# Optimization experiments

Hardware: AMD Instinct MI355X
Metric: run time of the kernel (lower is better)

## Reference

```python
import jax, jax.numpy as jnp
import numpy as np

EPS_COV = 1e-5


def svd_whiten(x):
    # x: (N, C, H, W) -> whitened (N, C, H*W), whitening matrix (N, C, C), mean (N, C, 1)
    N, C, H, W = x.shape
    xf = x.reshape(N, C, H * W)
    mean = xf.mean(-1, keepdims=True)
    xc = xf - mean
    cov = jnp.einsum('nch,ndh->ncd', xc, xc) / (H * W - 1) + EPS_COV * jnp.eye(C, dtype=x.dtype)
    # SVD of symmetric PSD cov; wm = U diag(e^-1/2) U^T (sign-invariant)
    u, e, _ = jnp.linalg.svd(cov)
    wm = jnp.einsum('nij,nj,nkj->nik', u, 1.0 / jnp.sqrt(e), u)
    whitened = jnp.einsum('ncd,ndh->nch', wm, xc)
    return whitened, wm, mean


def randomize_texture(wm, eps):
    # wm: (B, C, C); eps: (B, C, C) standard normal noise
    B, C, _ = wm.shape
    eye = jnp.eye(C, dtype=wm.dtype)
    triu_mask = jnp.triu(jnp.ones((C, C), dtype=wm.dtype))  # includes diagonal
    wm_trid = wm * (1.0 - triu_mask)  # strictly lower triangle, zeros elsewhere
    num_tri = C * (C - 1) / 2.0
    trid_mean = wm_trid.sum((1, 2)) / num_tri  # (B,)
    # NOTE: faithful to source -- the (C*C - num_tri) structural zeros contribute
    # (0 - mean)^2 terms, and divisor is num_tri.
    trid_std = jnp.sqrt(((wm_trid - trid_mean[:, None, None]) ** 2).sum((1, 2)) / num_tri)
    wm_samp = trid_mean[:, None, None] + 10.0 * trid_std[:, None, None] * eps  # torch.normal(mean, 10*std)
    triu_new = wm_samp * triu_mask
    trid_new = jnp.swapaxes(triu_new, 1, 2)
    diag_new = jnp.diagonal(wm_samp, axis1=1, axis2=2)  # (B, C)
    diag_orig = jnp.diagonal(wm, axis1=1, axis2=2)
    wm_new = triu_new + trid_new - 2.0 * eye * diag_new[:, :, None] + eye * diag_orig[:, :, None]
    return wm_new


def reference(x, eps):
    N, C, H, W = x.shape
    # avg_pool2d(x, 2) then nearest upsample back to (H, W): exact 2x2 block mean repeat
    pooled = x.reshape(N, C, H // 2, 2, W // 2, 2).mean(axis=(3, 5))
    up = jnp.repeat(jnp.repeat(pooled, 2, axis=2), 2, axis=3)
    HH = x - up
    LL = up
    cont_min = jnp.min(LL)
    cont_max = jnp.max(LL)
    whiten_cF, wm_c, c_mean = svd_whiten(LL)
    wm_s = randomize_texture(wm_c, eps)
    # torch.bmm(torch.inverse(wm_s), whiten_cF) == solve(wm_s, whiten_cF)
    target = jnp.linalg.solve(wm_s, whiten_cF)  # (N, C, H*W)
    target = target.reshape(N, C, H, W) + c_mean.reshape(N, C, 1, 1)
    target = jnp.clip(target, cont_min, cont_max)
    return HH + target


def setup_inputs() -> dict:
    key = jax.random.key(0)
    k1, k2 = jax.random.split(key)
    x = jax.random.normal(k1, (8, 256, 128, 128), dtype=jnp.float32)
    eps = jax.random.normal(k2, (8, 256, 256), dtype=jnp.float32)
    return {"x": x, "eps": eps}
```

## Files before the change

kernel.cpp:

```cpp
#include <hip/hip_runtime.h>
#include <math.h>

#define N_B   8
#define C_DIM 256
#define H_DIM 128
#define W_DIM 128
#define HW    (H_DIM*W_DIM)
#define PH    64
#define PW    64
#define PHW   (PH*PW)
#define CC    (C_DIM*C_DIM)
#define EPS_COV 1e-5f
#define COVSCALE (4.0f / 16383.0f)
#define NBGJ 16
#define PGLD 33

__device__ inline unsigned int fenc(float f) {
    unsigned int u = __float_as_uint(f);
    return (u & 0x80000000u) ? ~u : (u | 0x80000000u);
}
__device__ inline float fdec(unsigned int u) {
    return (u & 0x80000000u) ? __uint_as_float(u & 0x7fffffffu) : __uint_as_float(~u);
}

__global__ void pool_kernel(const float* __restrict__ x, float* __restrict__ p,
                            float* __restrict__ mean, float* __restrict__ sqb,
                            unsigned int* __restrict__ mm)
{
    int nc = blockIdx.x;
    int t  = threadIdx.x;
    const float* xp = x + (size_t)nc * HW;
    float* pp = p + (size_t)nc * PHW;
    float lsum = 0.f, lsq = 0.f, lmin = 1e30f, lmax = -1e30f;
    #pragma unroll
    for (int i = 0; i < PHW/256; ++i) {
        int pidx = i*256 + t;
        int ph = pidx >> 6, pw = pidx & 63;
        const float* r0 = xp + (size_t)(2*ph)*W_DIM + 2*pw;
        float2 a = *reinterpret_cast<const float2*>(r0);
        float2 b = *reinterpret_cast<const float2*>(r0 + W_DIM);
        float v = (a.x + a.y + b.x + b.y) * 0.25f;
        pp[pidx] = v;
        lsum += v;
        lsq  += v * v;
        lmin = fminf(lmin, v);
        lmax = fmaxf(lmax, v);
    }
    __shared__ float ssum[256], ssq[256], smin[256], smax[256];
    ssum[t] = lsum; ssq[t] = lsq; smin[t] = lmin; smax[t] = lmax;
    __syncthreads();
    for (int s = 128; s > 0; s >>= 1) {
        if (t < s) {
            ssum[t] += ssum[t+s];
            ssq[t]  += ssq[t+s];
            smin[t] = fminf(smin[t], smin[t+s]);
            smax[t] = fmaxf(smax[t], smax[t+s]);
        }
        __syncthreads();
    }
    if (t == 0) {
        mean[nc] = ssum[0] / (float)PHW;
        sqb[nc]  = ssq[0];
        atomicMin(&mm[0], fenc(smin[0]));
        atomicMax(&mm[1], fenc(smax[0]));
    }
}

__global__ void cvec_kernel(const float* __restrict__ mean, const float* __restrict__ sqb,
                            float* __restrict__ cvec, float* __restrict__ scv)
{
    int b = blockIdx.x, t = threadIdx.x;
    float m = mean[b*C_DIM + t];
    float s2 = sqb[b*C_DIM + t];
    float cv = COVSCALE * (s2 - (float)PHW * m * m) + EPS_COV;
    __shared__ float s[256];
    s[t] = cv; __syncthreads();
    for (int st = 128; st > 0; st >>= 1) {
        if (t < st) s[t] += s[t+st];
        __syncthreads();
    }
    if (t == 0) {
        float c = s[0] / 256.0f;
        cvec[b] = c;
        scv[b] = 1.0f / sqrtf(c);
    }
}

__global__ void cov_part_kernel(const float* __restrict__ p, const float* __restrict__ mean,
                                float* __restrict__ c0p, float* __restrict__ c1p,
                                float* __restrict__ c2p, float* __restrict__ c3p)
{
    int bx = blockIdx.x, by = blockIdx.y;
    if (bx > by) return;
    int bz = blockIdx.z;
    int b  = bz >> 2, ks = bz & 3;
    float* covp = (ks == 0) ? c0p : (ks == 1) ? c1p : (ks == 2) ? c2p : c3p;
    int c0 = bx * 64, d0 = by * 64;
    int t  = threadIdx.x;
    int tx = t & 15, ty = t >> 4;
    __shared__ float As[16][68];
    __shared__ float Bs[16][68];
    const float* pb = p + (size_t)b * C_DIM * PHW;
    const float* mb = mean + b * C_DIM;
    int lr  = t >> 2;
    int lc4 = (t & 3) * 4;
    float am = mb[c0 + lr];
    float bm = mb[d0 + lr];
    const float* aptr = pb + (size_t)(c0 + lr) * PHW + ks*1024 + lc4;
    const float* bptr = pb + (size_t)(d0 + lr) * PHW + ks*1024 + lc4;
    float acc[4][4] = {};
    for (int k0 = 0; k0 < 1024; k0 += 16) {
        float4 av = *reinterpret_cast<const float4*>(aptr + k0);
        float4 bv = *reinterpret_cast<const float4*>(bptr + k0);
        __syncthreads();
        As[lc4+0][lr] = av.x - am; As[lc4+1][lr] = av.y - am;
        As[lc4+2][lr] = av.z - am; As[lc4+3][lr] = av.w - am;
        Bs[lc4+0][lr] = bv.x - bm; Bs[lc4+1][lr] = bv.y - bm;
        Bs[lc4+2][lr] = bv.z - bm; Bs[lc4+3][lr] = bv.w - bm;
        __syncthreads();
        #pragma unroll
        for (int kk = 0; kk < 16; ++kk) {
            float4 a4 = *reinterpret_cast<const float4*>(&As[kk][ty*4]);
            float4 b4 = *reinterpret_cast<const float4*>(&Bs[kk][tx*4]);
            float a[4] = {a4.x, a4.y, a4.z, a4.w};
            float bb[4] = {b4.x, b4.y, b4.z, b4.w};
            #pragma unroll
            for (int i = 0; i < 4; ++i)
                #pragma unroll
                for (int j = 0; j < 4; ++j)
                    acc[i][j] += a[i] * bb[j];
        }
    }
    float* cb = covp + (size_t)b * CC;
    #pragma unroll
    for (int i = 0; i < 4; ++i) {
        int ci = c0 + ty*4 + i;
        #pragma unroll
        for (int j = 0; j < 4; ++j) {
            int dj = d0 + tx*4 + j;
            cb[(size_t)ci * C_DIM + dj] = acc[i][j];
            cb[(size_t)dj * C_DIM + ci] = acc[i][j];
        }
    }
}

__global__ void combine_kernel(const float* __restrict__ c0p, const float* __restrict__ c1p,
                               const float* __restrict__ c2p, const float* __restrict__ c3p,
                               const float* __restrict__ cvec,
                               float* __restrict__ Y, float* __restrict__ W0)
{
    size_t idx = (size_t)blockIdx.x * 256 + threadIdx.x;
    int b  = (int)(idx >> 16);
    int ij = (int)(idx & 65535);
    int diag = ((ij >> 8) == (ij & 255));
    float s = (c0p[idx] + c1p[idx] + c2p[idx] + c3p[idx]) * COVSCALE;
    float covv = s + (diag ? EPS_COV : 0.0f);
    float y = covv * (1.0f / cvec[b]);
    Y[idx] = y;
    W0[idx] = (diag ? 1.5f : 0.0f) - 0.5f * y;
}

__device__ inline void tile64(const float* __restrict__ Ab, int lda,
                              const float* __restrict__ Bb, int ldb,
                              int n, int r0, int c0, int t,
                              float (&As)[16][68], float (&Bs)[16][68],
                              float (&acc)[4][4])
{
    int tx = t & 15, ty = t >> 4;
    int lr = t >> 2, lc4 = (t & 3) * 4;
    int brow = t >> 4, bcol = (t & 15) * 4;
    for (int k0 = 0; k0 < n; k0 += 16) {
        float4 av = *reinterpret_cast<const float4*>(Ab + (size_t)(r0+lr)*lda + k0 + lc4);
        float4 bv = *reinterpret_cast<const float4*>(Bb + (size_t)(k0+brow)*ldb + c0 + bcol);
        __syncthreads();
        As[lc4+0][lr] = av.x; As[lc4+1][lr] = av.y; As[lc4+2][lr] = av.z; As[lc4+3][lr] = av.w;
        *reinterpret_cast<float4*>(&Bs[brow][bcol]) = bv;
        __syncthreads();
        #pragma unroll
        for (int kk = 0; kk < 16; ++kk) {
            float4 a4 = *reinterpret_cast<const float4*>(&As[kk][ty*4]);
            float4 b4 = *reinterpret_cast<const float4*>(&Bs[kk][tx*4]);
            float a[4] = {a4.x, a4.y, a4.z, a4.w};
            float bb[4] = {b4.x, b4.y, b4.z, b4.w};
            #pragma unroll
            for (int i = 0; i < 4; ++i)
                #pragma unroll
                for (int j = 0; j < 4; ++j)
                    acc[i][j] += a[i] * bb[j];
        }
    }
}

__global__ void gemm_kernel(const float* __restrict__ A, int lda, long long sA,
                            const float* __restrict__ B, int ldb, long long sB,
                            float* __restrict__ C, int ldc, long long sC,
                            const float* __restrict__ Cin, int ldcin, long long sCin,
                            const float* __restrict__ alphav,
                            int n, float alpha, float beta, float gamma)
{
    int b  = blockIdx.z;
    int r0 = blockIdx.x * 64, c0 = blockIdx.y * 64;
    int t  = threadIdx.x;
    int tx = t & 15, ty = t >> 4;
    __shared__ float As[16][68];
    __shared__ float Bs[16][68];
    float acc[4][4] = {};
    tile64(A + (size_t)b*sA, lda, B + (size_t)b*sB, ldb, n, r0, c0, t, As, Bs, acc);
    float al = alpha * (alphav ? alphav[b] : 1.0f);
    float* Cb = C + (size_t)b * sC;
    #pragma unroll
    for (int i = 0; i < 4; ++i) {
        int r = r0 + ty*4 + i;
        #pragma unroll
        for (int j = 0; j < 4; ++j) {
            int c = c0 + tx*4 + j;
            float v = al * acc[i][j];
            if (beta != 0.0f && r == c) v += beta;
            if (gamma != 0.0f) v += gamma * Cin[(size_t)b*sCin + (size_t)r*ldcin + c];
            Cb[(size_t)r*ldc + c] = v;
        }
    }
}

__global__ void ns_pair_kernel(const float* __restrict__ Y, const float* __restrict__ Z,
                               const float* __restrict__ W,
                               float* __restrict__ Yn, float* __restrict__ Zn)
{
    int bz = blockIdx.z;
    int b = bz >> 1, which = bz & 1;
    const float* A = which ? W + (size_t)b*CC : Y + (size_t)b*CC;
    const float* B = which ? Z + (size_t)b*CC : W + (size_t)b*CC;
    float*       C = which ? Zn + (size_t)b*CC : Yn + (size_t)b*CC;
    int r0 = blockIdx.x * 64, c0 = blockIdx.y * 64;
    int t  = threadIdx.x;
    int tx = t & 15, ty = t >> 4;
    __shared__ float As[16][68];
    __shared__ float Bs[16][68];
    float acc[4][4] = {};
    tile64(A, 256, B, 256, 256, r0, c0, t, As, Bs, acc);
    #pragma unroll
    for (int i = 0; i < 4; ++i)
        #pragma unroll
        for (int j = 0; j < 4; ++j)
            C[(size_t)(r0+ty*4+i)*256 + c0+tx*4+j] = acc[i][j];
}

__global__ void tex_partial_kernel(const float* __restrict__ Zf,
                                   float* __restrict__ tsum, float* __restrict__ tsq)
{
    int bx = blockIdx.x;
    int b = bx >> 5, chunk = bx & 31;
    const float* w = Zf + (size_t)b * CC;
    int t = threadIdx.x;
    int base = chunk * 2048;
    float sum = 0.f, sq = 0.f;
    #pragma unroll
    for (int k = 0; k < 8; ++k) {
        int flat = base + k*256 + t;
        int i = flat >> 8, j = flat & 255;
        if (i > j) {
            float v = w[flat];
            sum += v; sq += v * v;
        }
    }
    __shared__ float s1[256], s2[256];
    s1[t] = sum; s2[t] = sq;
    __syncthreads();
    for (int st = 128; st > 0; st >>= 1) {
        if (t < st) { s1[t] += s1[t+st]; s2[t] += s2[t+st]; }
        __syncthreads();
    }
    if (t == 0) {
        atomicAdd(&tsum[b], s1[0]);
        atomicAdd(&tsq[b],  s2[0]);
    }
}

__global__ void assemble_kernel(const float* __restrict__ Zf, const float* __restrict__ scv,
                                const float* __restrict__ eps,
                                const float* __restrict__ tsum, const float* __restrict__ tsq,
                                float* __restrict__ wms)
{
    size_t idx = (size_t)blockIdx.x * 256 + threadIdx.x;
    int b  = (int)(idx >> 16);
    int ij = (int)(idx & 65535);
    int i = ij >> 8, j = ij & 255;
    float s = scv[b];
    float v;
    if (i == j) {
        v = Zf[idx] * s;
    } else {
        float sum = tsum[b] * s;
        float sq  = tsq[b] * s * s;
        float m = sum / 32640.0f;
        float var = (sq - 2.0f*m*sum + m*m*65536.0f) / 32640.0f;
        float sd = sqrtf(fmaxf(var, 0.0f));
        int lo = min(i, j), hi = max(i, j);
        v = m + 10.0f * sd * eps[(size_t)b*CC + (size_t)lo*256 + hi];
    }
    wms[idx] = v;
}

__global__ __launch_bounds__(256, 1)
void gj_inv128_kernel(const float* __restrict__ Ain, int lda, long long sA,
                      float* __restrict__ Out, int ldo, long long sO)
{
    __shared__ float PG[2][128][PGLD];
    __shared__ float Rs[NBGJ][256];
    __shared__ int   pivots[NBGJ];
    __shared__ int   rowdest[128];
    __shared__ int   used[128];
    __shared__ float sh_rp;
    __shared__ int   sh_p;

    int b = blockIdx.x;
    int t = threadIdx.x;
    int q = t & 15;
    int rg = t >> 4;
    const float* Ab = Ain + (size_t)b * sA;

    float Areg[8][16];
    #pragma unroll
    for (int rr = 0; rr < 8; ++rr) {
        int r = rg*8 + rr;
        #pragma unroll
        for (int cc = 0; cc < 16; ++cc) {
            int c = q + cc*16;
            Areg[rr][cc] = (c < 128) ? Ab[(size_t)r*lda + c]
                                     : ((c - 128 == r) ? 1.0f : 0.0f);
        }
    }
    if (t < 128) used[t] = 0;
    __syncthreads();

    for (int pb = 0; pb < 8; ++pb) {
        #pragma unroll
        for (int rr = 0; rr < 8; ++rr) {
            float val = 0.f;
            #pragma unroll
            for (int cc = 0; cc < 16; ++cc)
                if (cc == pb) val = Areg[rr][cc];
            PG[0][rg*8 + rr][q] = val;
            PG[0][rg*8 + rr][16 + q] = 0.f;
        }
        __syncthreads();

        #pragma unroll
        for (int j = 0; j < NBGJ; ++j) {
            const int cur = j & 1;
            if (t < 64) {
                float v1 = used[t]    ? -1.f : fabsf(PG[cur][t][j]);
                float v2 = used[t+64] ? -1.f : fabsf(PG[cur][t+64][j]);
                int i1 = t;
                if (v2 > v1) { v1 = v2; i1 = t + 64; }
                #pragma unroll
                for (int m = 32; m; m >>= 1) {
                    float ov = __shfl_xor(v1, m);
                    int   oi = __shfl_xor(i1, m);
                    if (ov > v1) { v1 = ov; i1 = oi; }
                }
                if (t == 0) {
                    sh_p = i1;
                    sh_rp = 1.0f / PG[cur][i1][j];
                    pivots[j] = i1;
                    rowdest[i1] = pb*NBGJ + j;
                    used[i1] = 1;
                }
            }
            __syncthreads();
            if (t < 128) {
                int p = sh_p; float rp = sh_rp;
                float f = PG[cur][t][j];
                float v = (t == p) ? (rp - 1.0f) : (-f * rp);
                #pragma unroll
                for (int jj = 0; jj < 32; ++jj) {
                    float nv = fmaf(v, PG[cur][p][jj], PG[cur][t][jj]);
                    PG[cur^1][t][jj] = (jj == 16 + j) ? v : nv;
                }
            }
            __syncthreads();
        }

        for (int j = 0; j < NBGJ; ++j) {
            int p = pivots[j];
            if ((p >> 3) == rg) {
                #pragma unroll
                for (int rr = 0; rr < 8; ++rr)
                    if ((p & 7) == rr) {
                        #pragma unroll
                        for (int cc = 0; cc < 16; ++cc)
                            Rs[j][q + cc*16] = Areg[rr][cc];
                    }
            }
        }
        __syncthreads();

        #pragma unroll
        for (int j = 0; j < NBGJ; ++j) {
            float rv[16];
            #pragma unroll
            for (int cc = 0; cc < 16; ++cc) rv[cc] = Rs[j][q + cc*16];
            #pragma unroll
            for (int rr = 0; rr < 8; ++rr) {
                float g = PG[0][rg*8 + rr][16 + j];
                #pragma unroll
                for (int cc = 0; cc < 16; ++cc)
                    Areg[rr][cc] = fmaf(g, rv[cc], Areg[rr][cc]);
            }
        }
        __syncthreads();
    }

    float* Ob = Out + (size_t)b * sO;
    #pragma unroll
    for (int rr = 0; rr < 8; ++rr) {
        int r = rg*8 + rr;
        int dest = rowdest[r];
        #pragma unroll
        for (int cc = 8; cc < 16; ++cc) {
            int c = q + cc*16;
            Ob[(size_t)dest*ldo + (c - 128)] = Areg[rr][cc];
        }
    }
}

__global__ void transpose128_kernel(const float* __restrict__ In, float* __restrict__ Outp)
{
    __shared__ float tile[16][17];
    int b = blockIdx.z;
    int r0 = blockIdx.y * 16, c0 = blockIdx.x * 16;
    int t = threadIdx.x;
    int tx = t & 15, ty = t >> 4;
    tile[ty][tx] = In[(size_t)b*CC + (size_t)(r0+ty)*256 + c0+tx];
    __syncthreads();
    Outp[(size_t)b*CC + (size_t)(c0+ty)*256 + r0+tx] = tile[tx][ty];
}

__global__ void target_kernel(const float* __restrict__ M, const float* __restrict__ p,
                              const float* __restrict__ mean, const float* __restrict__ x,
                              const unsigned int* __restrict__ mm, float* __restrict__ out)
{
    int b  = blockIdx.z;
    int c0 = blockIdx.x * 64;
    int ph = blockIdx.y;
    int h0 = ph * 64;
    int t  = threadIdx.x;
    int tx = t & 15, ty = t >> 4;
    __shared__ float As[16][68];
    __shared__ float Bs[16][68];
    __shared__ float accS[64][66];
    const float* Mb = M + (size_t)b * CC;
    const float* pb = p + (size_t)b * C_DIM * PHW;
    const float* mb = mean + b * C_DIM;
    int lr   = t >> 2;
    int lc4  = (t & 3) * 4;
    int brow = t >> 4;
    int bcol = (t & 15) * 4;
    float acc[4][4] = {};
    for (int k0 = 0; k0 < C_DIM; k0 += 16) {
        float4 av = *reinterpret_cast<const float4*>(Mb + (size_t)(c0+lr)*C_DIM + k0 + lc4);
        float  bm = mb[k0 + brow];
        float4 bv = *reinterpret_cast<const float4*>(pb + (size_t)(k0+brow)*PHW + h0 + bcol);
        bv.x -= bm; bv.y -= bm; bv.z -= bm; bv.w -= bm;
        __syncthreads();
        As[lc4+0][lr] = av.x; As[lc4+1][lr] = av.y; As[lc4+2][lr] = av.z; As[lc4+3][lr] = av.w;
        *reinterpret_cast<float4*>(&Bs[brow][bcol]) = bv;
        __syncthreads();
        #pragma unroll
        for (int kk = 0; kk < 16; ++kk) {
            float4 a4 = *reinterpret_cast<const float4*>(&As[kk][ty*4]);
            float4 b4 = *reinterpret_cast<const float4*>(&Bs[kk][tx*4]);
            float a[4] = {a4.x, a4.y, a4.z, a4.w};
            float bb[4] = {b4.x, b4.y, b4.z, b4.w};
            #pragma unroll
            for (int i = 0; i < 4; ++i)
                #pragma unroll
                for (int j = 0; j < 4; ++j)
                    acc[i][j] += a[i] * bb[j];
        }
    }
    __syncthreads();
    #pragma unroll
    for (int i = 0; i < 4; ++i)
        *reinterpret_cast<float4*>(&accS[ty*4+i][tx*4]) =
            make_float4(acc[i][0], acc[i][1], acc[i][2], acc[i][3]);
    __syncthreads();
    float mn = fdec(mm[0]);
    float mx = fdec(mm[1]);
    int lane_ch = t >> 5;
    int col4 = (t & 31) * 4;
    int pw2 = (t & 31) * 2;
    #pragma unroll
    for (int cc8 = 0; cc8 < 64; cc8 += 8) {
        int ch  = cc8 + lane_ch;
        int gch = c0 + ch;
        float me = mb[gch];
        float2 av = *reinterpret_cast<const float2*>(&accS[ch][pw2]);
        float t0 = fminf(fmaxf(av.x + me, mn), mx);
        float t1 = fminf(fmaxf(av.y + me, mn), mx);
        float2 pv = *reinterpret_cast<const float2*>(
            pb + (size_t)gch * PHW + h0 + pw2);
        size_t xbase = (((size_t)b * C_DIM + gch) * H_DIM + 2*ph) * W_DIM + col4;
        #pragma unroll
        for (int row = 0; row < 2; ++row) {
            float4 xv = *reinterpret_cast<const float4*>(x + xbase + row*W_DIM);
            float4 o;
            o.x = xv.x - pv.x + t0;
            o.y = xv.y - pv.x + t0;
            o.z = xv.z - pv.y + t1;
            o.w = xv.w - pv.y + t1;
            *reinterpret_cast<float4*>(out + xbase + row*W_DIM) = o;
        }
    }
}

extern "C" void kernel_launch(void* const* d_in, const int* in_sizes, int n_in,
                              void* d_out, int out_size, void* d_ws, size_t ws_size,
                              hipStream_t stream)
{
    const float* x   = (const float*)d_in[0];
    const float* eps = (const float*)d_in[1];
    float* out = (float*)d_out;
    float* w = (float*)d_ws;

    size_t o = 0;
    float* p    = w + o; o += (size_t)N_B * C_DIM * PHW;
    float* bufA = w + o; o += (size_t)N_B * CC;
    float* bufY = w + o; o += (size_t)N_B * CC;
    float* bufZ = w + o; o += (size_t)N_B * CC;
    float* bufY2= w + o; o += (size_t)N_B * CC;
    float* bufZ2= w + o; o += (size_t)N_B * CC;
    float* bufW = w + o; o += (size_t)N_B * CC;
    float* bufT = w + o; o += (size_t)N_B * CC;
    float* meanb= w + o; o += N_B * C_DIM;
    float* sqb  = w + o; o += N_B * C_DIM;
    float* cvec = w + o; o += N_B;
    float* scv  = w + o; o += N_B;
    float* tsum = w + o; o += N_B;
    float* tsq  = w + o; o += N_B;
    unsigned int* mmx = (unsigned int*)(w + o); o += 2;

    float* wms  = bufA;
    float* covp0 = bufY2, *covp1 = bufZ, *covp2 = bufZ2, *covp3 = bufT;
    float* invA11 = bufW;
    float* T1     = bufW + (size_t)N_B * 128 * 128;
    float* Sm     = bufW + (size_t)N_B * 128 * 128 * 2;
    float* Minv   = bufY2;
    float* Rb     = bufZ;
    float* Minv2  = bufY;
    float* Mm     = bufT;

    hipMemsetAsync(mmx,     0xFF, 4, stream);
    hipMemsetAsync(mmx + 1, 0x00, 4, stream);
    hipMemsetAsync(tsum, 0, 2 * N_B * sizeof(float), stream);

    pool_kernel<<<N_B * C_DIM, 256, 0, stream>>>(x, p, meanb, sqb, mmx);
    cvec_kernel<<<N_B, 256, 0, stream>>>(meanb, sqb, cvec, scv);
    cov_part_kernel<<<dim3(4, 4, N_B*4), 256, 0, stream>>>(p, meanb, covp0, covp1, covp2, covp3);
    combine_kernel<<<2048, 256, 0, stream>>>(covp0, covp1, covp2, covp3, cvec, bufY, bufW);

    const long long S  = (long long)CC;
    const long long Sh = 128LL * 128LL;

    gemm_kernel<<<dim3(4,4,N_B), 256, 0, stream>>>(bufY,256,S, bufW,256,S, bufY2,256,S,
                                                   nullptr,0,0, nullptr, 256, 1.0f, 0.0f, 0.0f);
    gemm_kernel<<<dim3(4,4,N_B), 256, 0, stream>>>(bufW,256,S, bufY2,256,S, bufY,256,S,
                                                   nullptr,0,0, nullptr, 256, -0.5f, 1.5f, 0.0f);
    ns_pair_kernel<<<dim3(4,4,2*N_B), 256, 0, stream>>>(bufY2, bufW, bufY, bufZ, bufZ2);
    gemm_kernel<<<dim3(4,4,N_B), 256, 0, stream>>>(bufZ2,256,S, bufZ,256,S, bufY2,256,S,
                                                   nullptr,0,0, nullptr, 256, -0.5f, 1.5f, 0.0f);
    ns_pair_kernel<<<dim3(4,4,2*N_B), 256, 0, stream>>>(bufZ, bufZ2, bufY2, bufW, bufY);
    gemm_kernel<<<dim3(4,4,N_B), 256, 0, stream>>>(bufY,256,S, bufW,256,S, bufZ,256,S,
                                                   nullptr,0,0, nullptr, 256, -0.5f, 1.5f, 0.0f);
    gemm_kernel<<<dim3(4,4,N_B), 256, 0, stream>>>(bufZ,256,S, bufY,256,S, bufZ2,256,S,
                                                   nullptr,0,0, nullptr, 256, 1.0f, 0.0f, 0.0f);

    tex_partial_kernel<<<256, 256, 0, stream>>>(bufZ2, tsum, tsq);
    assemble_kernel<<<2048, 256, 0, stream>>>(bufZ2, scv, eps, tsum, tsq, wms);

    gj_inv128_kernel<<<N_B, 256, 0, stream>>>(wms, 256, S, invA11, 128, Sh);
    gemm_kernel<<<dim3(2,2,N_B), 256, 0, stream>>>(invA11,128,Sh, wms+128,256,S, T1,128,Sh,
                                                   nullptr,0,0, nullptr, 128, 1.0f, 0.0f, 0.0f);
    gemm_kernel<<<dim3(2,2,N_B), 256, 0, stream>>>(wms+128*256,256,S, T1,128,Sh, Sm,128,Sh,
                                                   wms+128*256+128,256,S, nullptr, 128, -1.0f, 0.0f, 1.0f);
    gj_inv128_kernel<<<N_B, 256, 0, stream>>>(Sm, 128, Sh, Minv+128*256+128, 256, S);
    gemm_kernel<<<dim3(2,2,N_B), 256, 0, stream>>>(T1,128,Sh, Minv+128*256+128,256,S, Minv+128,256,S,
                                                   nullptr,0,0, nullptr, 128, -1.0f, 0.0f, 0.0f);
    transpose128_kernel<<<dim3(8,8,N_B), 256, 0, stream>>>(Minv+128, Minv+128*256);
    gemm_kernel<<<dim3(2,2,N_B), 256, 0, stream>>>(T1,128,Sh, Minv+128*256,256,S, Minv,256,S,
                                                   invA11,128,Sh, nullptr, 128, -1.0f, 0.0f, 1.0f);
    gemm_kernel<<<dim3(4,4,N_B), 256, 0, stream>>>(wms,256,S, Minv,256,S, Rb,256,S,
                                                   nullptr,0,0, nullptr, 256, -1.0f, 2.0f, 0.0f);
    gemm_kernel<<<dim3(4,4,N_B), 256, 0, stream>>>(Minv,256,S, Rb,256,S, Minv2,256,S,
                                                   nullptr,0,0, nullptr, 256, 1.0f, 0.0f, 0.0f);
    gemm_kernel<<<dim3(4,4,N_B), 256, 0, stream>>>(Minv2,256,S, bufZ2,256,S, Mm,256,S,
                                                   nullptr,0,0, scv, 256, 1.0f, 0.0f, 0.0f);

    target_kernel<<<dim3(4, 64, N_B), 256, 0, stream>>>(Mm, p, meanb, x, mmx, out);

    (void)in_sizes; (void)n_in; (void)out_size; (void)ws_size;
}
```

Baseline: 989.2 us.

## Factor Gauss-Jordan panel inside a single wavefront using registers and shuffles

The per-column pivot search and panel elimination in the 128x128 Gauss-Jordan inverse now run inside one 64-lane wavefront. Each lane holds two panel rows in registers, and pivot rows are broadcast with shuffles. This removes the two block-wide barriers per pivot column and the shared-memory ping-pong buffer. Pivot selection packs the magnitude and row index into one integer key, which truncates the low mantissa bits and can change tie-breaking. The cost is higher register pressure and idle lanes while the panel is factored.

```diff
diff --git a/kernel.cpp b/kernel.cpp
--- a/kernel.cpp
+++ b/kernel.cpp
@@ -13,7 +13,6 @@
 #define EPS_COV 1e-5f
 #define COVSCALE (4.0f / 16383.0f)
 #define NBGJ 16
-#define PGLD 33
 
 __device__ inline unsigned int fenc(float f) {
     unsigned int u = __float_as_uint(f);
@@ -305,18 +304,17 @@
 void gj_inv128_kernel(const float* __restrict__ Ain, int lda, long long sA,
                       float* __restrict__ Out, int ldo, long long sO)
 {
-    __shared__ float PG[2][128][PGLD];
+    __shared__ float Pnl[128][17];
+    __shared__ float Gl[128][17];
     __shared__ float Rs[NBGJ][256];
     __shared__ int   pivots[NBGJ];
     __shared__ int   rowdest[128];
-    __shared__ int   used[128];
-    __shared__ float sh_rp;
-    __shared__ int   sh_p;
 
     int b = blockIdx.x;
     int t = threadIdx.x;
     int q = t & 15;
     int rg = t >> 4;
+    int lane = t & 63;
     const float* Ab = Ain + (size_t)b * sA;
 
     float Areg[8][16];
@@ -330,8 +328,7 @@
                                      : ((c - 128 == r) ? 1.0f : 0.0f);
         }
     }
-    if (t < 128) used[t] = 0;
-    __syncthreads();
+    int used0 = 0, used1 = 0, dest0 = 0, dest1 = 0, pvkeep = 0;
 
     for (int pb = 0; pb < 8; ++pb) {
         #pragma unroll
@@ -340,46 +337,73 @@
             #pragma unroll
             for (int cc = 0; cc < 16; ++cc)
                 if (cc == pb) val = Areg[rr][cc];
-            PG[0][rg*8 + rr][q] = val;
-            PG[0][rg*8 + rr][16 + q] = 0.f;
-        }
-        __syncthreads();
-
-        #pragma unroll
-        for (int j = 0; j < NBGJ; ++j) {
-            const int cur = j & 1;
-            if (t < 64) {
-                float v1 = used[t]    ? -1.f : fabsf(PG[cur][t][j]);
-                float v2 = used[t+64] ? -1.f : fabsf(PG[cur][t+64][j]);
-                int i1 = t;
-                if (v2 > v1) { v1 = v2; i1 = t + 64; }
+            Pnl[rg*8 + rr][q] = val;
+        }
+        __syncthreads();
+
+        if (t < 64) {
+            float pan0[16], pan1[16], g0[16], g1[16];
+            #pragma unroll
+            for (int cc = 0; cc < 16; ++cc) {
+                pan0[cc] = Pnl[lane][cc];
+                pan1[cc] = Pnl[lane + 64][cc];
+                g0[cc] = 0.f; g1[cc] = 0.f;
+            }
+            #pragma unroll
+            for (int j = 0; j < NBGJ; ++j) {
+                unsigned k0 = used0 ? 0u :
+                    ((__float_as_uint(fabsf(pan0[j])) & 0xFFFFFF80u) | (unsigned)lane);
+                unsigned k1 = used1 ? 0u :
+                    ((__float_as_uint(fabsf(pan1[j])) & 0xFFFFFF80u) | (unsigned)(lane + 64));
+                unsigned k = k0 > k1 ? k0 : k1;
                 #pragma unroll
                 for (int m = 32; m; m >>= 1) {
-                    float ov = __shfl_xor(v1, m);
-                    int   oi = __shfl_xor(i1, m);
-                    if (ov > v1) { v1 = ov; i1 = oi; }
+                    unsigned ok = __shfl_xor(k, m);
+                    if (ok > k) k = ok;
                 }
-                if (t == 0) {
-                    sh_p = i1;
-                    sh_rp = 1.0f / PG[cur][i1][j];
-                    pivots[j] = i1;
-                    rowdest[i1] = pb*NBGJ + j;
-                    used[i1] = 1;
+                int p = (int)(k & 127u);
+                int srcl = p & 63, hi = p >> 6;
+                float pj[16];
+                #pragma unroll
+                for (int cc = 0; cc < 16; ++cc) {
+                    float tmp = hi ? pan1[cc] : pan0[cc];
+                    pj[cc] = __shfl(tmp, srcl);
                 }
+                float gj[16];
+                #pragma unroll
+                for (int cc = 0; cc < 16; ++cc) {
+                    if (cc < j) {
+                        float tg = hi ? g1[cc] : g0[cc];
+                        gj[cc] = __shfl(tg, srcl);
+                    }
+                }
+                float rp = 1.0f / pj[j];
+                int isp0 = (lane == srcl) && (hi == 0);
+                int isp1 = (lane == srcl) && (hi == 1);
+                float v0 = isp0 ? (rp - 1.0f) : (-pan0[j] * rp);
+                float v1 = isp1 ? (rp - 1.0f) : (-pan1[j] * rp);
+                #pragma unroll
+                for (int cc = 0; cc < 16; ++cc) {
+                    pan0[cc] = fmaf(v0, pj[cc], pan0[cc]);
+                    pan1[cc] = fmaf(v1, pj[cc], pan1[cc]);
+                    if (cc < j) {
+                        g0[cc] = fmaf(v0, gj[cc], g0[cc]);
+                        g1[cc] = fmaf(v1, gj[cc], g1[cc]);
+                    }
+                }
+                g0[j] = v0; g1[j] = v1;
+                if (isp0) { used0 = 1; dest0 = pb*NBGJ + j; }
+                if (isp1) { used1 = 1; dest1 = pb*NBGJ + j; }
+                if (lane == j) pvkeep = p;
             }
-            __syncthreads();
-            if (t < 128) {
-                int p = sh_p; float rp = sh_rp;
-                float f = PG[cur][t][j];
-                float v = (t == p) ? (rp - 1.0f) : (-f * rp);
-                #pragma unroll
-                for (int jj = 0; jj < 32; ++jj) {
-                    float nv = fmaf(v, PG[cur][p][jj], PG[cur][t][jj]);
-                    PG[cur^1][t][jj] = (jj == 16 + j) ? v : nv;
-                }
+            #pragma unroll
+            for (int cc = 0; cc < 16; ++cc) {
+                Gl[lane][cc]      = g0[cc];
+                Gl[lane + 64][cc] = g1[cc];
             }
-            __syncthreads();
-        }
+            if (lane < NBGJ) pivots[lane] = pvkeep;
+        }
+        __syncthreads();
 
         for (int j = 0; j < NBGJ; ++j) {
             int p = pivots[j];
@@ -402,7 +426,7 @@
             for (int cc = 0; cc < 16; ++cc) rv[cc] = Rs[j][q + cc*16];
             #pragma unroll
             for (int rr = 0; rr < 8; ++rr) {
-                float g = PG[0][rg*8 + rr][16 + j];
+                float g = Gl[rg*8 + rr][j];
                 #pragma unroll
                 for (int cc = 0; cc < 16; ++cc)
                     Areg[rr][cc] = fmaf(g, rv[cc], Areg[rr][cc]);
@@ -410,6 +434,9 @@
         }
         __syncthreads();
     }
+
+    if (t < 64) { rowdest[lane] = dest0; rowdest[lane + 64] = dest1; }
+    __syncthreads();
 
     float* Ob = Out + (size_t)b * sO;
     #pragma unroll
```

After: 826.8 us. 1.2x faster.
